# Optimization experiments

Measured on AMD Instinct MI355X. Metric: run time of the kernel, lower is better.

Reference implementation:

```python
import jax, jax.numpy as jnp
import numpy as np

RANK = 16
ALPHA = 32
SCALING = ALPHA / RANK  # 2.0


def setup_inputs() -> dict:
    key = jax.random.key(0)
    k1, k2, k3 = jax.random.split(key, 3)
    B_, S, D, O = 2, 4096, 4096, 4096
    x = jax.random.normal(k1, (B_, S, D), dtype=jnp.float32)
    # Dequantized base weight, torch Linear layout [out, in]
    W_base = jax.random.normal(k2, (O, D), dtype=jnp.float32) * 0.02
    # kaiming_uniform-ish init for lora_A [rank, in]
    bound = float(np.sqrt(6.0 / (1 + 5) / D))
    A = jax.random.uniform(k3, (RANK, D), dtype=jnp.float32, minval=-bound, maxval=bound)
    # lora_B initialized to zeros [out, rank]
    Bm = jnp.zeros((O, RANK), dtype=jnp.float32)
    return {"x": x, "W_base": W_base, "A": A, "B": Bm}


def reference(x, W_base, A, B):
    # Y = x @ W_base^T + (x @ A^T) @ B^T * scaling   (dropout p=0 -> identity)
    base_out = jnp.einsum('bsd,od->bso', x, W_base)
    lora_mid = jnp.einsum('bsd,rd->bsr', x, A)        # [B,S,rank]
    lora_out = jnp.einsum('bsr,or->bso', lora_mid, B) # [B,S,out]
    return base_out + lora_out * SCALING
```

## Files before the change

### kernel.cpp

```cpp
#include <hip/hip_runtime.h>
#include <hip/hip_bf16.h>

typedef __attribute__((ext_vector_type(8))) __bf16 bf16x8;
typedef __attribute__((ext_vector_type(4))) float  f32x4;

__global__ __launch_bounds__(256) void cvt_f32_bf16(
    const float* __restrict__ in, __bf16* __restrict__ out, long n8)
{
    long i = (long)blockIdx.x * blockDim.x + threadIdx.x;
    long stride = (long)gridDim.x * blockDim.x;
    for (; i < n8; i += stride) {
        const f32x4* p = (const f32x4*)(in + i * 8);
        f32x4 a = p[0], b = p[1];
        bf16x8 o;
        o[0] = (__bf16)a[0]; o[1] = (__bf16)a[1];
        o[2] = (__bf16)a[2]; o[3] = (__bf16)a[3];
        o[4] = (__bf16)b[0]; o[5] = (__bf16)b[1];
        o[6] = (__bf16)b[2]; o[7] = (__bf16)b[3];
        *(bf16x8*)(out + i * 8) = o;
    }
}

__global__ __launch_bounds__(256) void mid_and_cvt(
    const float* __restrict__ x, const float* __restrict__ A,
    float* __restrict__ mid, __bf16* __restrict__ Xb, int K, int M)
{
    int tid = threadIdx.x;
    int m0 = blockIdx.x * 4;

    float acc[4][16];
#pragma unroll
    for (int row = 0; row < 4; ++row)
#pragma unroll
        for (int r = 0; r < 16; ++r) acc[row][r] = 0.f;

    int iters = K / 2048;
    for (int it = 0; it < iters; ++it) {
        int k = it * 2048 + tid * 8;
        f32x4 xv[4][2];
#pragma unroll
        for (int row = 0; row < 4; ++row) {
            if (m0 + row < M) {
                const float* xr = x + (size_t)(m0 + row) * K;
                xv[row][0] = *(const f32x4*)(xr + k);
                xv[row][1] = *(const f32x4*)(xr + k + 4);
            } else {
                f32x4 z = {0.f,0.f,0.f,0.f};
                xv[row][0] = z; xv[row][1] = z;
            }
            if (Xb && m0 + row < M) {
                bf16x8 o;
                o[0] = (__bf16)xv[row][0][0]; o[1] = (__bf16)xv[row][0][1];
                o[2] = (__bf16)xv[row][0][2]; o[3] = (__bf16)xv[row][0][3];
                o[4] = (__bf16)xv[row][1][0]; o[5] = (__bf16)xv[row][1][1];
                o[6] = (__bf16)xv[row][1][2]; o[7] = (__bf16)xv[row][1][3];
                *(bf16x8*)(Xb + (size_t)(m0 + row) * K + k) = o;
            }
        }
#pragma unroll
        for (int r = 0; r < 16; ++r) {
            const f32x4* ap = (const f32x4*)(A + (size_t)r * K + k);
            f32x4 a0 = ap[0], a1 = ap[1];
#pragma unroll
            for (int row = 0; row < 4; ++row) {
                acc[row][r] += xv[row][0][0]*a0[0] + xv[row][0][1]*a0[1]
                             + xv[row][0][2]*a0[2] + xv[row][0][3]*a0[3]
                             + xv[row][1][0]*a1[0] + xv[row][1][1]*a1[1]
                             + xv[row][1][2]*a1[2] + xv[row][1][3]*a1[3];
            }
        }
    }

#pragma unroll
    for (int row = 0; row < 4; ++row)
#pragma unroll
        for (int r = 0; r < 16; ++r)
#pragma unroll
            for (int off = 32; off > 0; off >>= 1)
                acc[row][r] += __shfl_down(acc[row][r], off, 64);

    __shared__ float red[4][4][16];
    int lane = tid & 63, w = tid >> 6;
    if (lane == 0) {
#pragma unroll
        for (int row = 0; row < 4; ++row)
#pragma unroll
            for (int r = 0; r < 16; ++r) red[w][row][r] = acc[row][r];
    }
    __syncthreads();
    if (tid < 64) {
        int row = tid >> 4, r = tid & 15;
        if (m0 + row < M) {
            float s = red[0][row][r] + red[1][row][r]
                    + red[2][row][r] + red[3][row][r];
            mid[(size_t)(m0 + row) * 16 + r] = s;
        }
    }
}

#define GL16(g, l) __builtin_amdgcn_global_load_lds( \
    (const __attribute__((address_space(1))) void*)(g), \
    (__attribute__((address_space(3))) void*)(l), 16, 0, 0)

#define DSR(dst, addr, IMM) \
    asm volatile("ds_read_b128 %0, %1 offset:" IMM : "=v"(dst) : "v"(addr))

#define BAR()   __builtin_amdgcn_s_barrier()
#define LGKM0() asm volatile("s_waitcnt lgkmcnt(0)" ::: )
#define SCHED() __builtin_amdgcn_sched_barrier(0)

__global__ __launch_bounds__(512, 2) void gemm256(
    const __bf16* __restrict__ Xb,
    const __bf16* __restrict__ Wb,
    const float*  __restrict__ mid,
    const float*  __restrict__ Bl,
    float* __restrict__ out,
    int M, int N, int K)
{
    __shared__ __bf16 As[4][256 * 32];
    __shared__ __bf16 Bs[4][256 * 32];

    const int NT = K >> 5;

    int nbx = N >> 8, nby = M >> 8, nwg = nbx * nby;
    int bid = blockIdx.x, swz = bid;
    if ((nwg & 7) == 0) { int cpx = nwg >> 3; swz = (bid & 7) * cpx + (bid >> 3); }
    int by = swz / nbx, bx = swz % nbx;
    int m0 = by << 8, n0 = bx << 8;

    int tid = threadIdx.x;
    int lane = tid & 63;
    int w = tid >> 6;
    int wm = w >> 2, wn = w & 3;

    int q0 = tid >> 2;
    int c0 = tid & 3;
    int csrc = c0 ^ ((q0 >> 1) & 3);
    const __bf16* sA0 = Xb + (size_t)(m0 + q0) * K + csrc * 8;
    const __bf16* sA1 = sA0 + (size_t)128 * K;
    const __bf16* sB0 = Wb + (size_t)(n0 + q0) * K + csrc * 8;
    const __bf16* sB1 = sB0 + (size_t)128 * K;
    unsigned ldsw = (unsigned)w * 1024;

    int chunkSwz = (lane >> 4) ^ ((lane >> 1) & 3);
    unsigned aoff = (unsigned)((wm * 128 + (lane & 15)) * 64 + chunkSwz * 16);
    unsigned boff = (unsigned)((wn * 64  + (lane & 15)) * 64 + chunkSwz * 16);

    unsigned a_addr = (unsigned)(size_t)(__attribute__((address_space(3))) __bf16*)&As[0][0] + aoff;
    unsigned b_addr = (unsigned)(size_t)(__attribute__((address_space(3))) __bf16*)&Bs[0][0] + boff;

#define STAGE_A(t, b) do { size_t ko = (size_t)(t) * 32; \
    GL16(sA0 + ko, (char*)As[b] + ldsw); \
    GL16(sA1 + ko, (char*)As[b] + 8192 + ldsw); } while (0)
#define STAGE_B(t, b) do { size_t ko = (size_t)(t) * 32; \
    GL16(sB0 + ko, (char*)Bs[b] + ldsw); \
    GL16(sB1 + ko, (char*)Bs[b] + 8192 + ldsw); } while (0)

    f32x4 acc[8][4];
    {
        int kh = lane >> 4;
        bf16x8 bI[4];
#pragma unroll
        for (int j = 0; j < 4; ++j) {
            bf16x8 v = {};
            if (kh < 2) {
                int col = n0 + wn * 64 + j * 16 + (lane & 15);
                const f32x4* p = (const f32x4*)(Bl + (size_t)col * 16 + kh * 8);
                f32x4 v0 = p[0], v1 = p[1];
                v[0] = (__bf16)(2.0f * v0[0]); v[1] = (__bf16)(2.0f * v0[1]);
                v[2] = (__bf16)(2.0f * v0[2]); v[3] = (__bf16)(2.0f * v0[3]);
                v[4] = (__bf16)(2.0f * v1[0]); v[5] = (__bf16)(2.0f * v1[1]);
                v[6] = (__bf16)(2.0f * v1[2]); v[7] = (__bf16)(2.0f * v1[3]);
            }
            bI[j] = v;
        }
#pragma unroll
        for (int i = 0; i < 8; ++i) {
            bf16x8 aI = {};
            if (kh < 2) {
                int row = m0 + wm * 128 + i * 16 + (lane & 15);
                const f32x4* p = (const f32x4*)(mid + (size_t)row * 16 + kh * 8);
                f32x4 v0 = p[0], v1 = p[1];
                aI[0] = (__bf16)v0[0]; aI[1] = (__bf16)v0[1];
                aI[2] = (__bf16)v0[2]; aI[3] = (__bf16)v0[3];
                aI[4] = (__bf16)v1[0]; aI[5] = (__bf16)v1[1];
                aI[6] = (__bf16)v1[2]; aI[7] = (__bf16)v1[3];
            }
            f32x4 z = {0.f, 0.f, 0.f, 0.f};
#pragma unroll
            for (int j = 0; j < 4; ++j)
                acc[i][j] = __builtin_amdgcn_mfma_f32_16x16x32_bf16(aI, bI[j], z, 0, 0, 0);
        }
    }

    STAGE_A(0, 0); STAGE_B(0, 0);
    STAGE_A(1, 1); STAGE_B(1, 1);
    asm volatile("s_waitcnt vmcnt(4)" ::: "memory");
    BAR();

    bf16x8 axf0, axf1, axf2, axf3, bxf0, bxf1, bxf2, bxf3;
    bf16x8 ayf0, ayf1, ayf2, ayf3, byf0, byf1, byf2, byf3;
    bf16x8 ax4, ax5, ax6, ax7, ay4, ay5, ay6, ay7;

    DSR(axf0, a_addr, "0");    DSR(axf1, a_addr, "1024");
    DSR(axf2, a_addr, "2048"); DSR(axf3, a_addr, "3072");
    DSR(bxf0, b_addr, "0");    DSR(bxf1, b_addr, "1024");
    DSR(bxf2, b_addr, "2048"); DSR(bxf3, b_addr, "3072");

    for (int t = 0; t < NT; t += 2) {
        unsigned aT0 = a_addr + ((unsigned)(t & 3) << 14);
        unsigned aT1 = a_addr + ((unsigned)((t + 1) & 3) << 14);
        unsigned bT1 = b_addr + ((unsigned)((t + 1) & 3) << 14);
        unsigned aT2 = a_addr + ((unsigned)((t + 2) & 3) << 14);
        unsigned bT2 = b_addr + ((unsigned)((t + 2) & 3) << 14);
        bool p2 = (t + 2) < NT;
        bool p3 = (t + 3) < NT;

        if (p2) STAGE_A(t + 2, (t + 2) & 3);
        BAR();
        LGKM0();
        SCHED();
        DSR(ax4, aT0, "4096"); DSR(ax5, aT0, "5120");
        DSR(ax6, aT0, "6144"); DSR(ax7, aT0, "7168");
        SCHED();
        __builtin_amdgcn_s_setprio(1);
        acc[0][0] = __builtin_amdgcn_mfma_f32_16x16x32_bf16(axf0, bxf0, acc[0][0], 0, 0, 0);
        acc[0][1] = __builtin_amdgcn_mfma_f32_16x16x32_bf16(axf0, bxf1, acc[0][1], 0, 0, 0);
        acc[0][2] = __builtin_amdgcn_mfma_f32_16x16x32_bf16(axf0, bxf2, acc[0][2], 0, 0, 0);
        acc[0][3] = __builtin_amdgcn_mfma_f32_16x16x32_bf16(axf0, bxf3, acc[0][3], 0, 0, 0);
        acc[1][0] = __builtin_amdgcn_mfma_f32_16x16x32_bf16(axf1, bxf0, acc[1][0], 0, 0, 0);
        acc[1][1] = __builtin_amdgcn_mfma_f32_16x16x32_bf16(axf1, bxf1, acc[1][1], 0, 0, 0);
        acc[1][2] = __builtin_amdgcn_mfma_f32_16x16x32_bf16(axf1, bxf2, acc[1][2], 0, 0, 0);
        acc[1][3] = __builtin_amdgcn_mfma_f32_16x16x32_bf16(axf1, bxf3, acc[1][3], 0, 0, 0);
        acc[2][0] = __builtin_amdgcn_mfma_f32_16x16x32_bf16(axf2, bxf0, acc[2][0], 0, 0, 0);
        acc[2][1] = __builtin_amdgcn_mfma_f32_16x16x32_bf16(axf2, bxf1, acc[2][1], 0, 0, 0);
        acc[2][2] = __builtin_amdgcn_mfma_f32_16x16x32_bf16(axf2, bxf2, acc[2][2], 0, 0, 0);
        acc[2][3] = __builtin_amdgcn_mfma_f32_16x16x32_bf16(axf2, bxf3, acc[2][3], 0, 0, 0);
        acc[3][0] = __builtin_amdgcn_mfma_f32_16x16x32_bf16(axf3, bxf0, acc[3][0], 0, 0, 0);
        acc[3][1] = __builtin_amdgcn_mfma_f32_16x16x32_bf16(axf3, bxf1, acc[3][1], 0, 0, 0);
        acc[3][2] = __builtin_amdgcn_mfma_f32_16x16x32_bf16(axf3, bxf2, acc[3][2], 0, 0, 0);
        acc[3][3] = __builtin_amdgcn_mfma_f32_16x16x32_bf16(axf3, bxf3, acc[3][3], 0, 0, 0);
        __builtin_amdgcn_s_setprio(0);

        if (p2) {
            STAGE_B(t + 2, (t + 2) & 3);
            asm volatile("s_waitcnt vmcnt(4)" ::: "memory");
        } else {
            asm volatile("s_waitcnt vmcnt(0)" ::: "memory");
        }
        BAR();
        LGKM0();
        SCHED();
        DSR(ayf0, aT1, "0");    DSR(ayf1, aT1, "1024");
        DSR(ayf2, aT1, "2048"); DSR(ayf3, aT1, "3072");
        DSR(byf0, bT1, "0");    DSR(byf1, bT1, "1024");
        DSR(byf2, bT1, "2048"); DSR(byf3, bT1, "3072");
        SCHED();
        __builtin_amdgcn_s_setprio(1);
        acc[4][0] = __builtin_amdgcn_mfma_f32_16x16x32_bf16(ax4, bxf0, acc[4][0], 0, 0, 0);
        acc[4][1] = __builtin_amdgcn_mfma_f32_16x16x32_bf16(ax4, bxf1, acc[4][1], 0, 0, 0);
        acc[4][2] = __builtin_amdgcn_mfma_f32_16x16x32_bf16(ax4, bxf2, acc[4][2], 0, 0, 0);
        acc[4][3] = __builtin_amdgcn_mfma_f32_16x16x32_bf16(ax4, bxf3, acc[4][3], 0, 0, 0);
        acc[5][0] = __builtin_amdgcn_mfma_f32_16x16x32_bf16(ax5, bxf0, acc[5][0], 0, 0, 0);
        acc[5][1] = __builtin_amdgcn_mfma_f32_16x16x32_bf16(ax5, bxf1, acc[5][1], 0, 0, 0);
        acc[5][2] = __builtin_amdgcn_mfma_f32_16x16x32_bf16(ax5, bxf2, acc[5][2], 0, 0, 0);
        acc[5][3] = __builtin_amdgcn_mfma_f32_16x16x32_bf16(ax5, bxf3, acc[5][3], 0, 0, 0);
        acc[6][0] = __builtin_amdgcn_mfma_f32_16x16x32_bf16(ax6, bxf0, acc[6][0], 0, 0, 0);
        acc[6][1] = __builtin_amdgcn_mfma_f32_16x16x32_bf16(ax6, bxf1, acc[6][1], 0, 0, 0);
        acc[6][2] = __builtin_amdgcn_mfma_f32_16x16x32_bf16(ax6, bxf2, acc[6][2], 0, 0, 0);
        acc[6][3] = __builtin_amdgcn_mfma_f32_16x16x32_bf16(ax6, bxf3, acc[6][3], 0, 0, 0);
        acc[7][0] = __builtin_amdgcn_mfma_f32_16x16x32_bf16(ax7, bxf0, acc[7][0], 0, 0, 0);
        acc[7][1] = __builtin_amdgcn_mfma_f32_16x16x32_bf16(ax7, bxf1, acc[7][1], 0, 0, 0);
        acc[7][2] = __builtin_amdgcn_mfma_f32_16x16x32_bf16(ax7, bxf2, acc[7][2], 0, 0, 0);
        acc[7][3] = __builtin_amdgcn_mfma_f32_16x16x32_bf16(ax7, bxf3, acc[7][3], 0, 0, 0);
        __builtin_amdgcn_s_setprio(0);

        if (p3) STAGE_A(t + 3, (t + 3) & 3);
        BAR();
        LGKM0();
        SCHED();
        DSR(ay4, aT1, "4096"); DSR(ay5, aT1, "5120");
        DSR(ay6, aT1, "6144"); DSR(ay7, aT1, "7168");
        SCHED();
        __builtin_amdgcn_s_setprio(1);
        acc[0][0] = __builtin_amdgcn_mfma_f32_16x16x32_bf16(ayf0, byf0, acc[0][0], 0, 0, 0);
        acc[0][1] = __builtin_amdgcn_mfma_f32_16x16x32_bf16(ayf0, byf1, acc[0][1], 0, 0, 0);
        acc[0][2] = __builtin_amdgcn_mfma_f32_16x16x32_bf16(ayf0, byf2, acc[0][2], 0, 0, 0);
        acc[0][3] = __builtin_amdgcn_mfma_f32_16x16x32_bf16(ayf0, byf3, acc[0][3], 0, 0, 0);
        acc[1][0] = __builtin_amdgcn_mfma_f32_16x16x32_bf16(ayf1, byf0, acc[1][0], 0, 0, 0);
        acc[1][1] = __builtin_amdgcn_mfma_f32_16x16x32_bf16(ayf1, byf1, acc[1][1], 0, 0, 0);
        acc[1][2] = __builtin_amdgcn_mfma_f32_16x16x32_bf16(ayf1, byf2, acc[1][2], 0, 0, 0);
        acc[1][3] = __builtin_amdgcn_mfma_f32_16x16x32_bf16(ayf1, byf3, acc[1][3], 0, 0, 0);
        acc[2][0] = __builtin_amdgcn_mfma_f32_16x16x32_bf16(ayf2, byf0, acc[2][0], 0, 0, 0);
        acc[2][1] = __builtin_amdgcn_mfma_f32_16x16x32_bf16(ayf2, byf1, acc[2][1], 0, 0, 0);
        acc[2][2] = __builtin_amdgcn_mfma_f32_16x16x32_bf16(ayf2, byf2, acc[2][2], 0, 0, 0);
        acc[2][3] = __builtin_amdgcn_mfma_f32_16x16x32_bf16(ayf2, byf3, acc[2][3], 0, 0, 0);
        acc[3][0] = __builtin_amdgcn_mfma_f32_16x16x32_bf16(ayf3, byf0, acc[3][0], 0, 0, 0);
        acc[3][1] = __builtin_amdgcn_mfma_f32_16x16x32_bf16(ayf3, byf1, acc[3][1], 0, 0, 0);
        acc[3][2] = __builtin_amdgcn_mfma_f32_16x16x32_bf16(ayf3, byf2, acc[3][2], 0, 0, 0);
        acc[3][3] = __builtin_amdgcn_mfma_f32_16x16x32_bf16(ayf3, byf3, acc[3][3], 0, 0, 0);
        __builtin_amdgcn_s_setprio(0);

        if (p3) {
            STAGE_B(t + 3, (t + 3) & 3);
            asm volatile("s_waitcnt vmcnt(4)" ::: "memory");
        } else {
            asm volatile("s_waitcnt vmcnt(0)" ::: "memory");
        }
        BAR();
        LGKM0();
        SCHED();
        if (p2) {
            DSR(axf0, aT2, "0");    DSR(axf1, aT2, "1024");
            DSR(axf2, aT2, "2048"); DSR(axf3, aT2, "3072");
            DSR(bxf0, bT2, "0");    DSR(bxf1, bT2, "1024");
            DSR(bxf2, bT2, "2048"); DSR(bxf3, bT2, "3072");
        }
        SCHED();
        __builtin_amdgcn_s_setprio(1);
        acc[4][0] = __builtin_amdgcn_mfma_f32_16x16x32_bf16(ay4, byf0, acc[4][0], 0, 0, 0);
        acc[4][1] = __builtin_amdgcn_mfma_f32_16x16x32_bf16(ay4, byf1, acc[4][1], 0, 0, 0);
        acc[4][2] = __builtin_amdgcn_mfma_f32_16x16x32_bf16(ay4, byf2, acc[4][2], 0, 0, 0);
        acc[4][3] = __builtin_amdgcn_mfma_f32_16x16x32_bf16(ay4, byf3, acc[4][3], 0, 0, 0);
        acc[5][0] = __builtin_amdgcn_mfma_f32_16x16x32_bf16(ay5, byf0, acc[5][0], 0, 0, 0);
        acc[5][1] = __builtin_amdgcn_mfma_f32_16x16x32_bf16(ay5, byf1, acc[5][1], 0, 0, 0);
        acc[5][2] = __builtin_amdgcn_mfma_f32_16x16x32_bf16(ay5, byf2, acc[5][2], 0, 0, 0);
        acc[5][3] = __builtin_amdgcn_mfma_f32_16x16x32_bf16(ay5, byf3, acc[5][3], 0, 0, 0);
        acc[6][0] = __builtin_amdgcn_mfma_f32_16x16x32_bf16(ay6, byf0, acc[6][0], 0, 0, 0);
        acc[6][1] = __builtin_amdgcn_mfma_f32_16x16x32_bf16(ay6, byf1, acc[6][1], 0, 0, 0);
        acc[6][2] = __builtin_amdgcn_mfma_f32_16x16x32_bf16(ay6, byf2, acc[6][2], 0, 0, 0);
        acc[6][3] = __builtin_amdgcn_mfma_f32_16x16x32_bf16(ay6, byf3, acc[6][3], 0, 0, 0);
        acc[7][0] = __builtin_amdgcn_mfma_f32_16x16x32_bf16(ay7, byf0, acc[7][0], 0, 0, 0);
        acc[7][1] = __builtin_amdgcn_mfma_f32_16x16x32_bf16(ay7, byf1, acc[7][1], 0, 0, 0);
        acc[7][2] = __builtin_amdgcn_mfma_f32_16x16x32_bf16(ay7, byf2, acc[7][2], 0, 0, 0);
        acc[7][3] = __builtin_amdgcn_mfma_f32_16x16x32_bf16(ay7, byf3, acc[7][3], 0, 0, 0);
        __builtin_amdgcn_s_setprio(0);
    }

#pragma unroll
    for (int i = 0; i < 8; ++i) {
        int rbase = m0 + wm * 128 + i * 16 + ((lane >> 4) << 2);
#pragma unroll
        for (int q = 0; q < 4; ++q) {
            float* orow = out + (size_t)(rbase + q) * N;
            int colb = n0 + wn * 64 + (lane & 15);
            orow[colb]      = acc[i][0][q];
            orow[colb + 16] = acc[i][1][q];
            orow[colb + 32] = acc[i][2][q];
            orow[colb + 48] = acc[i][3][q];
        }
    }
}

__global__ __launch_bounds__(256) void gemm_fb(
    const float* __restrict__ X, const float* __restrict__ W,
    const float* __restrict__ mid, const float* __restrict__ Bl,
    float* __restrict__ out, int M, int N, int K)
{
    __shared__ float As[64][16];
    __shared__ float Bs[64][16];
    int nbx = N / 64;
    int bx = blockIdx.x % nbx, by = blockIdx.x / nbx;
    int m0 = by * 64, n0 = bx * 64;
    int tid = threadIdx.x;
    int tr = tid >> 4, tc = tid & 15;

    float acc[4][4] = {};
    for (int kt = 0; kt < K; kt += 16) {
#pragma unroll
        for (int s = 0; s < 4; ++s) {
            int c = s * 256 + tid;
            int row = c >> 4, kk = c & 15;
            As[row][kk] = X[(size_t)(m0 + row) * K + kt + kk];
            Bs[row][kk] = W[(size_t)(n0 + row) * K + kt + kk];
        }
        __syncthreads();
#pragma unroll
        for (int kk = 0; kk < 16; ++kk) {
            float av[4], bv[4];
#pragma unroll
            for (int i = 0; i < 4; ++i) { av[i] = As[tr*4+i][kk]; bv[i] = Bs[tc*4+i][kk]; }
#pragma unroll
            for (int i = 0; i < 4; ++i)
#pragma unroll
                for (int j = 0; j < 4; ++j) acc[i][j] += av[i] * bv[j];
        }
        __syncthreads();
    }
#pragma unroll
    for (int i = 0; i < 4; ++i) {
        int row = m0 + tr * 4 + i;
#pragma unroll
        for (int j = 0; j < 4; ++j) {
            int col = n0 + tc * 4 + j;
            float s = 0.f;
#pragma unroll
            for (int r = 0; r < 16; ++r)
                s += mid[(size_t)row * 16 + r] * Bl[(size_t)col * 16 + r];
            out[(size_t)row * N + col] = acc[i][j] + 2.0f * s;
        }
    }
}

extern "C" void kernel_launch(void* const* d_in, const int* in_sizes, int n_in,
                              void* d_out, int out_size, void* d_ws, size_t ws_size,
                              hipStream_t stream)
{
    const float* x   = (const float*)d_in[0];
    const float* Wf  = (const float*)d_in[1];
    const float* A   = (const float*)d_in[2];
    const float* Bl  = (const float*)d_in[3];
    float* out = (float*)d_out;

    int D = in_sizes[2] / 16;
    int O = in_sizes[3] / 16;
    long M = (long)in_sizes[0] / D;
    int K = D, N = O;

    size_t xb_bytes  = (size_t)M * K * 2;
    size_t wb_bytes  = (size_t)N * K * 2;
    size_t mid_bytes = (size_t)M * 16 * 4;

    bool shapes_ok = (M % 256 == 0) && (N % 256 == 0) && (K % 2048 == 0);

    int midgrid = (int)((M + 3) / 4);

    if (shapes_ok && ws_size >= xb_bytes + wb_bytes + mid_bytes) {
        __bf16* Xb  = (__bf16*)d_ws;
        __bf16* Wbb = (__bf16*)((char*)d_ws + xb_bytes);
        float*  mid = (float*)((char*)d_ws + xb_bytes + wb_bytes);

        cvt_f32_bf16<<<2048, 256, 0, stream>>>(Wf, Wbb, (long)N * K / 8);
        mid_and_cvt<<<midgrid, 256, 0, stream>>>(x, A, mid, Xb, K, (int)M);
        int nwg = (int)(M / 256) * (N / 256);
        gemm256<<<nwg, 512, 0, stream>>>(Xb, Wbb, mid, Bl, out, (int)M, N, K);
    } else {
        float* mid = (float*)d_ws;
        mid_and_cvt<<<midgrid, 256, 0, stream>>>(x, A, mid, nullptr, K, (int)M);
        int nwg = (int)(M / 64) * (N / 64);
        gemm_fb<<<nwg, 256, 0, stream>>>(x, Wf, mid, Bl, out, (int)M, N, K);
    }
}
```

Baseline: 331.6 us.

## Merge preprocessing kernels and deepen GEMM prefetch to four-stage lookahead

Fuses the weight bf16 conversion and the x conversion plus LoRA-mid computation into one launch that splits its blocks between the two jobs, which removes a launch and lets both run at the same time. The main GEMM now prefills all four LDS buffers and issues loads for tiles t+4 and t+5 in the middle of each iteration, with graded vmcnt waits, so global loads have more time in flight. The trade-off is more outstanding memory ops and a stricter shape requirement (K/32 >= 8). The fallback path now calls a separate mid-only kernel.

```diff
diff --git a/kernel.cpp b/kernel.cpp
--- a/kernel.cpp
+++ b/kernel.cpp
@@ -1,39 +1,112 @@
 #include <hip/hip_runtime.h>
 #include <hip/hip_bf16.h>
 
-typedef __attribute__((ext_vector_type(8))) __bf16 bf16x8;
-typedef __attribute__((ext_vector_type(4))) float  f32x4;
-
-__global__ __launch_bounds__(256) void cvt_f32_bf16(
-    const float* __restrict__ in, __bf16* __restrict__ out, long n8)
+typedef __attribute__((ext_vector_type(8)))  __bf16 bf16x8;
+typedef __attribute__((ext_vector_type(4)))  float  f32x4;
+
+__global__ __launch_bounds__(256) void preproc(
+    const float* __restrict__ x, const float* __restrict__ A,
+    const float* __restrict__ Wf,
+    float* __restrict__ mid, __bf16* __restrict__ Xb, __bf16* __restrict__ Wbb,
+    int K, int M, long nW8, int wBlocks)
 {
-    long i = (long)blockIdx.x * blockDim.x + threadIdx.x;
-    long stride = (long)gridDim.x * blockDim.x;
-    for (; i < n8; i += stride) {
-        const f32x4* p = (const f32x4*)(in + i * 8);
-        f32x4 a = p[0], b = p[1];
-        bf16x8 o;
-        o[0] = (__bf16)a[0]; o[1] = (__bf16)a[1];
-        o[2] = (__bf16)a[2]; o[3] = (__bf16)a[3];
-        o[4] = (__bf16)b[0]; o[5] = (__bf16)b[1];
-        o[6] = (__bf16)b[2]; o[7] = (__bf16)b[3];
-        *(bf16x8*)(out + i * 8) = o;
+    int tid = threadIdx.x;
+    if ((int)blockIdx.x < wBlocks) {
+        long i = (long)blockIdx.x * 256 + tid;
+        long stride = (long)wBlocks * 256;
+        for (; i < nW8; i += stride) {
+            const f32x4* p = (const f32x4*)(Wf + i * 8);
+            f32x4 a = p[0], b = p[1];
+            bf16x8 o;
+            o[0] = (__bf16)a[0]; o[1] = (__bf16)a[1];
+            o[2] = (__bf16)a[2]; o[3] = (__bf16)a[3];
+            o[4] = (__bf16)b[0]; o[5] = (__bf16)b[1];
+            o[6] = (__bf16)b[2]; o[7] = (__bf16)b[3];
+            *(bf16x8*)(Wbb + i * 8) = o;
+        }
+        return;
+    }
+
+    int m0 = ((int)blockIdx.x - wBlocks) * 4;
+    float acc[4][16];
+#pragma unroll
+    for (int row = 0; row < 4; ++row)
+#pragma unroll
+        for (int r = 0; r < 16; ++r) acc[row][r] = 0.f;
+
+    int iters = K / 2048;
+    for (int it = 0; it < iters; ++it) {
+        int k = it * 2048 + tid * 8;
+        f32x4 xv[4][2];
+#pragma unroll
+        for (int row = 0; row < 4; ++row) {
+            if (m0 + row < M) {
+                const float* xr = x + (size_t)(m0 + row) * K;
+                xv[row][0] = *(const f32x4*)(xr + k);
+                xv[row][1] = *(const f32x4*)(xr + k + 4);
+                bf16x8 o;
+                o[0] = (__bf16)xv[row][0][0]; o[1] = (__bf16)xv[row][0][1];
+                o[2] = (__bf16)xv[row][0][2]; o[3] = (__bf16)xv[row][0][3];
+                o[4] = (__bf16)xv[row][1][0]; o[5] = (__bf16)xv[row][1][1];
+                o[6] = (__bf16)xv[row][1][2]; o[7] = (__bf16)xv[row][1][3];
+                *(bf16x8*)(Xb + (size_t)(m0 + row) * K + k) = o;
+            } else {
+                f32x4 z = {0.f,0.f,0.f,0.f};
+                xv[row][0] = z; xv[row][1] = z;
+            }
+        }
+#pragma unroll
+        for (int r = 0; r < 16; ++r) {
+            const f32x4* ap = (const f32x4*)(A + (size_t)r * K + k);
+            f32x4 a0 = ap[0], a1 = ap[1];
+#pragma unroll
+            for (int row = 0; row < 4; ++row) {
+                acc[row][r] += xv[row][0][0]*a0[0] + xv[row][0][1]*a0[1]
+                             + xv[row][0][2]*a0[2] + xv[row][0][3]*a0[3]
+                             + xv[row][1][0]*a1[0] + xv[row][1][1]*a1[1]
+                             + xv[row][1][2]*a1[2] + xv[row][1][3]*a1[3];
+            }
+        }
+    }
+
+#pragma unroll
+    for (int row = 0; row < 4; ++row)
+#pragma unroll
+        for (int r = 0; r < 16; ++r)
+#pragma unroll
+            for (int off = 32; off > 0; off >>= 1)
+                acc[row][r] += __shfl_down(acc[row][r], off, 64);
+
+    __shared__ float red[4][4][16];
+    int lane = tid & 63, w = tid >> 6;
+    if (lane == 0) {
+#pragma unroll
+        for (int row = 0; row < 4; ++row)
+#pragma unroll
+            for (int r = 0; r < 16; ++r) red[w][row][r] = acc[row][r];
+    }
+    __syncthreads();
+    if (tid < 64) {
+        int row = tid >> 4, r = tid & 15;
+        if (m0 + row < M) {
+            float s = red[0][row][r] + red[1][row][r]
+                    + red[2][row][r] + red[3][row][r];
+            mid[(size_t)(m0 + row) * 16 + r] = s;
+        }
     }
 }
 
-__global__ __launch_bounds__(256) void mid_and_cvt(
+__global__ __launch_bounds__(256) void mid_only(
     const float* __restrict__ x, const float* __restrict__ A,
-    float* __restrict__ mid, __bf16* __restrict__ Xb, int K, int M)
+    float* __restrict__ mid, int K, int M)
 {
     int tid = threadIdx.x;
     int m0 = blockIdx.x * 4;
-
     float acc[4][16];
 #pragma unroll
     for (int row = 0; row < 4; ++row)
 #pragma unroll
         for (int r = 0; r < 16; ++r) acc[row][r] = 0.f;
-
     int iters = K / 2048;
     for (int it = 0; it < iters; ++it) {
         int k = it * 2048 + tid * 8;
@@ -48,14 +121,6 @@
                 f32x4 z = {0.f,0.f,0.f,0.f};
                 xv[row][0] = z; xv[row][1] = z;
             }
-            if (Xb && m0 + row < M) {
-                bf16x8 o;
-                o[0] = (__bf16)xv[row][0][0]; o[1] = (__bf16)xv[row][0][1];
-                o[2] = (__bf16)xv[row][0][2]; o[3] = (__bf16)xv[row][0][3];
-                o[4] = (__bf16)xv[row][1][0]; o[5] = (__bf16)xv[row][1][1];
-                o[6] = (__bf16)xv[row][1][2]; o[7] = (__bf16)xv[row][1][3];
-                *(bf16x8*)(Xb + (size_t)(m0 + row) * K + k) = o;
-            }
         }
 #pragma unroll
         for (int r = 0; r < 16; ++r) {
@@ -70,7 +135,6 @@
             }
         }
     }
-
 #pragma unroll
     for (int row = 0; row < 4; ++row)
 #pragma unroll
@@ -78,7 +142,6 @@
 #pragma unroll
             for (int off = 32; off > 0; off >>= 1)
                 acc[row][r] += __shfl_down(acc[row][r], off, 64);
-
     __shared__ float red[4][4][16];
     int lane = tid & 63, w = tid >> 6;
     if (lane == 0) {
@@ -108,6 +171,7 @@
 #define BAR()   __builtin_amdgcn_s_barrier()
 #define LGKM0() asm volatile("s_waitcnt lgkmcnt(0)" ::: )
 #define SCHED() __builtin_amdgcn_sched_barrier(0)
+#define VMW(n)  asm volatile("s_waitcnt vmcnt(" #n ")" ::: "memory")
 
 __global__ __launch_bounds__(512, 2) void gemm256(
     const __bf16* __restrict__ Xb,
@@ -142,19 +206,18 @@
     const __bf16* sB1 = sB0 + (size_t)128 * K;
     unsigned ldsw = (unsigned)w * 1024;
 
-    int chunkSwz = (lane >> 4) ^ ((lane >> 1) & 3);
-    unsigned aoff = (unsigned)((wm * 128 + (lane & 15)) * 64 + chunkSwz * 16);
-    unsigned boff = (unsigned)((wn * 64  + (lane & 15)) * 64 + chunkSwz * 16);
-
-    unsigned a_addr = (unsigned)(size_t)(__attribute__((address_space(3))) __bf16*)&As[0][0] + aoff;
-    unsigned b_addr = (unsigned)(size_t)(__attribute__((address_space(3))) __bf16*)&Bs[0][0] + boff;
-
 #define STAGE_A(t, b) do { size_t ko = (size_t)(t) * 32; \
     GL16(sA0 + ko, (char*)As[b] + ldsw); \
     GL16(sA1 + ko, (char*)As[b] + 8192 + ldsw); } while (0)
 #define STAGE_B(t, b) do { size_t ko = (size_t)(t) * 32; \
     GL16(sB0 + ko, (char*)Bs[b] + ldsw); \
     GL16(sB1 + ko, (char*)Bs[b] + 8192 + ldsw); } while (0)
+
+    int chunkSwz = (lane >> 4) ^ ((lane >> 1) & 3);
+    unsigned aoff = (unsigned)((wm * 128 + (lane & 15)) * 64 + chunkSwz * 16);
+    unsigned boff = (unsigned)((wn * 64  + (lane & 15)) * 64 + chunkSwz * 16);
+    unsigned a_addr = (unsigned)(size_t)(__attribute__((address_space(3))) __bf16*)&As[0][0] + aoff;
+    unsigned b_addr = (unsigned)(size_t)(__attribute__((address_space(3))) __bf16*)&Bs[0][0] + boff;
 
     f32x4 acc[8][4];
     {
@@ -195,7 +258,9 @@
 
     STAGE_A(0, 0); STAGE_B(0, 0);
     STAGE_A(1, 1); STAGE_B(1, 1);
-    asm volatile("s_waitcnt vmcnt(4)" ::: "memory");
+    STAGE_A(2, 2); STAGE_B(2, 2);
+    STAGE_A(3, 3); STAGE_B(3, 3);
+    VMW(12);
     BAR();
 
     bf16x8 axf0, axf1, axf2, axf3, bxf0, bxf1, bxf2, bxf3;
@@ -215,10 +280,11 @@
         unsigned bT2 = b_addr + ((unsigned)((t + 2) & 3) << 14);
         bool p2 = (t + 2) < NT;
         bool p3 = (t + 3) < NT;
-
-        if (p2) STAGE_A(t + 2, (t + 2) & 3);
+        bool p4 = (t + 4) < NT;
+        bool p5 = (t + 5) < NT;
+
+        LGKM0();
         BAR();
-        LGKM0();
         SCHED();
         DSR(ax4, aT0, "4096"); DSR(ax5, aT0, "5120");
         DSR(ax6, aT0, "6144"); DSR(ax7, aT0, "7168");
@@ -242,19 +308,17 @@
         acc[3][3] = __builtin_amdgcn_mfma_f32_16x16x32_bf16(axf3, bxf3, acc[3][3], 0, 0, 0);
         __builtin_amdgcn_s_setprio(0);
 
-        if (p2) {
-            STAGE_B(t + 2, (t + 2) & 3);
-            asm volatile("s_waitcnt vmcnt(4)" ::: "memory");
-        } else {
-            asm volatile("s_waitcnt vmcnt(0)" ::: "memory");
-        }
+        LGKM0();
+        if (p3)      { VMW(8); }
+        else if (p2) { VMW(4); }
+        else         { VMW(0); }
         BAR();
-        LGKM0();
         SCHED();
         DSR(ayf0, aT1, "0");    DSR(ayf1, aT1, "1024");
         DSR(ayf2, aT1, "2048"); DSR(ayf3, aT1, "3072");
         DSR(byf0, bT1, "0");    DSR(byf1, bT1, "1024");
         DSR(byf2, bT1, "2048"); DSR(byf3, bT1, "3072");
+        if (p4) { STAGE_A(t + 4, t & 3); STAGE_B(t + 4, t & 3); }
         SCHED();
         __builtin_amdgcn_s_setprio(1);
         acc[4][0] = __builtin_amdgcn_mfma_f32_16x16x32_bf16(ax4, bxf0, acc[4][0], 0, 0, 0);
@@ -275,9 +339,8 @@
         acc[7][3] = __builtin_amdgcn_mfma_f32_16x16x32_bf16(ax7, bxf3, acc[7][3], 0, 0, 0);
         __builtin_amdgcn_s_setprio(0);
 
-        if (p3) STAGE_A(t + 3, (t + 3) & 3);
+        LGKM0();
         BAR();
-        LGKM0();
         SCHED();
         DSR(ay4, aT1, "4096"); DSR(ay5, aT1, "5120");
         DSR(ay6, aT1, "6144"); DSR(ay7, aT1, "7168");
@@ -301,14 +364,11 @@
         acc[3][3] = __builtin_amdgcn_mfma_f32_16x16x32_bf16(ayf3, byf3, acc[3][3], 0, 0, 0);
         __builtin_amdgcn_s_setprio(0);
 
-        if (p3) {
-            STAGE_B(t + 3, (t + 3) & 3);
-            asm volatile("s_waitcnt vmcnt(4)" ::: "memory");
-        } else {
-            asm volatile("s_waitcnt vmcnt(0)" ::: "memory");
-        }
+        LGKM0();
+        if (p4)      { VMW(8); }
+        else if (p3) { VMW(4); }
+        else         { VMW(0); }
         BAR();
-        LGKM0();
         SCHED();
         if (p2) {
             DSR(axf0, aT2, "0");    DSR(axf1, aT2, "1024");
@@ -316,6 +376,7 @@
             DSR(bxf0, bT2, "0");    DSR(bxf1, bT2, "1024");
             DSR(bxf2, bT2, "2048"); DSR(bxf3, bT2, "3072");
         }
+        if (p5) { STAGE_A(t + 5, (t + 1) & 3); STAGE_B(t + 5, (t + 1) & 3); }
         SCHED();
         __builtin_amdgcn_s_setprio(1);
         acc[4][0] = __builtin_amdgcn_mfma_f32_16x16x32_bf16(ay4, byf0, acc[4][0], 0, 0, 0);
@@ -421,22 +482,25 @@
     size_t wb_bytes  = (size_t)N * K * 2;
     size_t mid_bytes = (size_t)M * 16 * 4;
 
-    bool shapes_ok = (M % 256 == 0) && (N % 256 == 0) && (K % 2048 == 0);
-
-    int midgrid = (int)((M + 3) / 4);
+    bool shapes_ok = (M % 256 == 0) && (N % 256 == 0) && (K % 2048 == 0)
+                     && (K / 32 >= 8);
+
+    int midBlocks = (int)((M + 3) / 4);
 
     if (shapes_ok && ws_size >= xb_bytes + wb_bytes + mid_bytes) {
         __bf16* Xb  = (__bf16*)d_ws;
         __bf16* Wbb = (__bf16*)((char*)d_ws + xb_bytes);
         float*  mid = (float*)((char*)d_ws + xb_bytes + wb_bytes);
 
-        cvt_f32_bf16<<<2048, 256, 0, stream>>>(Wf, Wbb, (long)N * K / 8);
-        mid_and_cvt<<<midgrid, 256, 0, stream>>>(x, A, mid, Xb, K, (int)M);
+        const int wBlocks = 1024;
+        long nW8 = (long)N * K / 8;
+        preproc<<<wBlocks + midBlocks, 256, 0, stream>>>(
+            x, A, Wf, mid, Xb, Wbb, K, (int)M, nW8, wBlocks);
         int nwg = (int)(M / 256) * (N / 256);
         gemm256<<<nwg, 512, 0, stream>>>(Xb, Wbb, mid, Bl, out, (int)M, N, K);
     } else {
         float* mid = (float*)d_ws;
-        mid_and_cvt<<<midgrid, 256, 0, stream>>>(x, A, mid, nullptr, K, (int)M);
+        mid_only<<<midBlocks, 256, 0, stream>>>(x, A, mid, K, (int)M);
         int nwg = (int)(M / 64) * (N / 64);
         gemm_fb<<<nwg, 256, 0, stream>>>(x, Wf, mid, Bl, out, (int)M, N, K);
     }
```

Result: no change. 330.6 us (-0.3%).
